# Performance work log

Measured on AMD Instinct MI355X. Metric: run time of the kernel, lower is better.

The kernel has to match this reference:

```python
import jax, jax.numpy as jnp
import numpy as np

G = 2            # num_codevector_groups
C = 320          # num_codevectors_per_group
VQ_DIM = 256     # codevector_dim
HID = 512        # conv_dimensions[-1]
TAU = 2.0


def setup_inputs() -> dict:
    key = jax.random.key(0)
    k1, k2, k3, k4 = jax.random.split(key, 4)
    B, S = 16, 2048
    x = jax.random.normal(k1, (B, S, HID), dtype=jnp.float32)
    # iid Gumbel(0,1) noise, same shape as flattened logits [B*S*G, C]
    u = jax.random.uniform(k2, (B * S * G, C), dtype=jnp.float32, minval=1e-6, maxval=1.0 - 1e-6)
    gumbel = -jnp.log(-jnp.log(u))
    Wq = jax.random.normal(k3, (G * C, HID), dtype=jnp.float32) * (1.0 / np.sqrt(HID))
    bq = jnp.zeros((G * C,), dtype=jnp.float32)
    codevectors = jax.random.uniform(k4, (1, G * C, VQ_DIM // G), dtype=jnp.float32)
    return {"x": x, "gumbel": gumbel, "Wq": Wq, "bq": bq, "codevectors": codevectors}


def reference(x, gumbel, Wq, bq, codevectors):
    B, S, H = x.shape
    N = B * S
    logits = jnp.einsum('bsh,gh->bsg', x, Wq) + bq          # [B, S, G*C]
    logits = logits.reshape(N * G, C)

    # hard gumbel-softmax (training path) with straight-through estimator
    y_soft = jax.nn.softmax((logits + gumbel) / TAU, axis=-1)
    idx = jnp.argmax(y_soft, axis=-1)
    y_hard = jax.nn.one_hot(idx, C, dtype=y_soft.dtype)
    probs = y_hard + y_soft - jax.lax.stop_gradient(y_soft)  # [N*G, C]

    # perplexity from plain softmax of logits (no gumbel noise), masked_token_idx=None
    soft_probs = jax.nn.softmax(logits.reshape(N, G, C), axis=-1)
    mean_p = soft_probs.mean(axis=0)                          # [G, C]
    perplexity = jnp.exp(-jnp.sum(mean_p * jnp.log(mean_p + 1e-7), axis=-1)).sum()

    # weighted sum over codes per group == einsum (same math as broadcast*sum in torch)
    cv = codevectors.reshape(G, C, VQ_DIM // G)               # [G, C, d]
    sel = jnp.einsum('ngc,gcd->ngd', probs.reshape(N, G, C), cv)
    selected_codes = sel.reshape(B, S, VQ_DIM)
    return selected_codes, perplexity
```

## Files before the change

kernel.cpp:

```cpp
#include <hip/hip_runtime.h>
#include <hip/hip_fp16.h>

#define HID 512
#define GC  640
#define CC  320
#define GG  2
#define DHALF 128
#define MARGIN 0.004f
#define FB 4
#define REPLD 324

typedef __attribute__((ext_vector_type(8))) _Float16 half8;
typedef __attribute__((ext_vector_type(4))) float float4v;

__device__ __forceinline__ void gload16(const void* g, void* l) {
    __builtin_amdgcn_global_load_lds(
        (const __attribute__((address_space(1))) void*)(unsigned long long)g,
        (__attribute__((address_space(3))) void*)(unsigned)(unsigned long long)l,
        16, 0, 0);
}

__global__ __launch_bounds__(256) void zero_misc(float* meanAcc, int* cnt) {
    for (int i = threadIdx.x; i < GC; i += 256) meanAcc[i] = 0.f;
    if (threadIdx.x < 2) cnt[threadIdx.x] = 0;
}

__global__ __launch_bounds__(256) void convert_f16(
    const float* __restrict__ in, unsigned short* __restrict__ out, int n8)
{
    int i = blockIdx.x * 256 + threadIdx.x;
    if (i >= n8) return;
    const float4* p = (const float4*)in + (size_t)i * 2;
    float4 v0 = p[0], v1 = p[1];
    float f[8] = {v0.x, v0.y, v0.z, v0.w, v1.x, v1.y, v1.z, v1.w};
    unsigned r[4];
#pragma unroll
    for (int j = 0; j < 4; ++j) {
        __half2 hh = __float22half2_rn(make_float2(f[2*j], f[2*j+1]));
        r[j] = __builtin_bit_cast(unsigned, hh);
    }
    uint4 o = {r[0], r[1], r[2], r[3]};
    *(uint4*)(out + (size_t)i * 8) = o;
}

__global__ __launch_bounds__(512, 4) void fused(
    const float* __restrict__ X, const unsigned short* __restrict__ Wh,
    const float* __restrict__ bq, const float* __restrict__ gum,
    const float* __restrict__ cv, float* __restrict__ out,
    float* __restrict__ meanAcc, int* __restrict__ cnt,
    int* __restrict__ flags0, int* __restrict__ flags1)
{
    __shared__ __align__(16) char lds[49152];
    unsigned short* As0 = (unsigned short*)lds;
    unsigned short* Bs0 = (unsigned short*)(lds + 8192);
    float* rep = (float*)lds;
    __shared__ float bqs[CC];
    __shared__ float smean[CC];

    const int tid  = threadIdx.x;
    const int lane = tid & 63;
    const int wid  = tid >> 6;
    const int wr   = wid >> 1;
    const int wc   = wid & 1;
    const int lq   = lane & 15;
    const int q    = lane >> 4;

    int bid = blockIdx.x, nwg = gridDim.x;
    int swz = ((nwg & 7) == 0) ? (bid & 7) * (nwg >> 3) + (bid >> 3) : bid;
    const int g    = swz & 1;
    const int tok0 = (swz >> 1) * 64;
    int* flagsg = g ? flags1 : flags0;

    for (int i = tid; i < CC; i += 512) { bqs[i] = bq[g * CC + i]; smean[i] = 0.f; }

    const int iss0 = wid, iss1 = wid + 8, iss2 = wid + 16;
    const int c0i = (iss0 * 64 + lane) ^ (((iss0 * 64 + lane) >> 3) & 7);
    const int c1i = (iss1 * 64 + lane) ^ (((iss1 * 64 + lane) >> 3) & 7);
    const int c2i = (iss2 * 64 + lane) ^ (((iss2 * 64 + lane) >> 3) & 7);
    const unsigned short* srcB0 = Wh + ((size_t)(g * CC + (c0i >> 2))) * HID + (c0i & 3) * 8;
    const unsigned short* srcB1 = Wh + ((size_t)(g * CC + (c1i >> 2))) * HID + (c1i & 3) * 8;
    const unsigned short* srcB2 = Wh + ((size_t)(g * CC + (c2i >> 2))) * HID + (c2i & 3) * 8;

    const int ca = tid ^ ((tid >> 3) & 7);
    const float* xsrc = X + (size_t)(tok0 + (ca >> 2)) * HID + (ca & 3) * 8;

    int aoff = ((wr * 16 + lq) << 6) + (q << 4);
    aoff ^= ((aoff >> 7) & 7) << 4;
    int boff = (lq << 6) + (q << 4);
    boff ^= ((lq >> 1) & 7) << 4;
    boff += wc * 10240;

    float4v acc[10];
#pragma unroll
    for (int j = 0; j < 10; ++j) acc[j] = (float4v){0.f, 0.f, 0.f, 0.f};

    if (tid < 256) {
        float4 xa = *(const float4*)xsrc;
        float4 xb = *(const float4*)(xsrc + 4);
        half8 h;
        h[0] = (_Float16)xa.x; h[1] = (_Float16)xa.y;
        h[2] = (_Float16)xa.z; h[3] = (_Float16)xa.w;
        h[4] = (_Float16)xb.x; h[5] = (_Float16)xb.y;
        h[6] = (_Float16)xb.z; h[7] = (_Float16)xb.w;
        *(half8*)&As0[tid * 8] = h;
    }
    gload16(srcB0, Bs0 + iss0 * 512);
    gload16(srcB1, Bs0 + iss1 * 512);
    if (wid < 4) gload16(srcB2, Bs0 + iss2 * 512);
    __syncthreads();

    int cur = 0;
    for (int kk = 0; kk < 16; ++kk) {
        const int k0n = ((kk + 1) & 15) * 32;
        float4 nxa = {}, nxb = {};
        if (tid < 256) {
            nxa = *(const float4*)(xsrc + k0n);
            nxb = *(const float4*)(xsrc + k0n + 4);
        }
        unsigned short* Bnext = Bs0 + (cur ^ 1) * 10240;
        gload16(srcB0 + k0n, Bnext + iss0 * 512);
        gload16(srcB1 + k0n, Bnext + iss1 * 512);
        if (wid < 4) gload16(srcB2 + k0n, Bnext + iss2 * 512);

        half8 a = *(const half8*)((const char*)(As0 + cur * 2048) + aoff);
        const char* bbase = (const char*)(Bs0 + cur * 10240) + boff;
#pragma unroll
        for (int j = 0; j < 10; ++j) {
            half8 b = *(const half8*)(bbase + j * 1024);
            acc[j] = __builtin_amdgcn_mfma_f32_16x16x32_f16(a, b, acc[j], 0, 0, 0);
        }

        if (tid < 256) {
            half8 h;
            h[0] = (_Float16)nxa.x; h[1] = (_Float16)nxa.y;
            h[2] = (_Float16)nxa.z; h[3] = (_Float16)nxa.w;
            h[4] = (_Float16)nxb.x; h[5] = (_Float16)nxb.y;
            h[6] = (_Float16)nxb.z; h[7] = (_Float16)nxb.w;
            *(half8*)&As0[(cur ^ 1) * 2048 + tid * 8] = h;
        }
        __syncthreads();
        cur ^= 1;
    }

    float macc[20];
#pragma unroll
    for (int j = 0; j < 20; ++j) macc[j] = 0.f;
    const int gg  = tid >> 4;
    const int lql = tid & 15;
    const int cb  = lql * 20;

    for (int r = 0; r < 4; ++r) {
        const int slot = wr * 4 + q;
#pragma unroll
        for (int j = 0; j < 10; ++j) {
            const int c = wc * 160 + j * 16 + lq;
            rep[slot * REPLD + c] = acc[j][r] + bqs[c];
        }
        __syncthreads();

        if (gg < 16) {
            const int rowL  = (gg >> 2) * 16 + (gg & 3) * 4 + r;
            const int tglob = tok0 + rowL;
            const float* grow = gum + ((size_t)tglob * GG + g) * CC + cb;
            const float* rrow = rep + gg * REPLD + cb;

            float s = 0.f;
            float b = -3.0e38f; int bi = 0; float s2 = -3.0e38f;
#pragma unroll
            for (int jj = 0; jj < 5; ++jj) {
                float4 lv = *(const float4*)(rrow + jj * 4);
                float4 gv = *(const float4*)(grow + jj * 4);
                float lf[4] = {lv.x, lv.y, lv.z, lv.w};
                float gf[4] = {gv.x, gv.y, gv.z, gv.w};
#pragma unroll
                for (int t = 0; t < 4; ++t) {
                    float v = lf[t] + gf[t];
                    if (v > b)       { s2 = b; b = v; bi = cb + jj * 4 + t; }
                    else if (v > s2) { s2 = v; }
                    s += __expf(lf[t]);
                }
            }
#pragma unroll
            for (int m = 1; m < 16; m <<= 1) {
                float os  = __shfl_xor(s,  m, 64);
                float ob  = __shfl_xor(b,  m, 64);
                int   obi = __shfl_xor(bi, m, 64);
                float os2 = __shfl_xor(s2, m, 64);
                s += os;
                if (ob > b || (ob == b && obi < bi)) { s2 = fmaxf(os2, b); b = ob; bi = obi; }
                else                                 { s2 = fmaxf(s2, ob); }
            }
            float inv = 1.f / s;
#pragma unroll
            for (int jj = 0; jj < 5; ++jj) {
                float4 lv = *(const float4*)(rrow + jj * 4);
                macc[jj*4+0] += __expf(lv.x) * inv;
                macc[jj*4+1] += __expf(lv.y) * inv;
                macc[jj*4+2] += __expf(lv.z) * inv;
                macc[jj*4+3] += __expf(lv.w) * inv;
            }

            if (lql == 0 && (b - s2) < MARGIN) {
                int p = atomicAdd(&cnt[g], 1);
                flagsg[p] = tglob;
            }
            const float* cvp = cv + ((size_t)(g * CC + bi)) * DHALF + lql * 8;
            float4 c0v = *(const float4*)cvp;
            float4 c1v = *(const float4*)(cvp + 4);
            float* op = out + (size_t)tglob * 256 + g * DHALF + lql * 8;
            *(float4*)op       = c0v;
            *(float4*)(op + 4) = c1v;
        }
        __syncthreads();
    }

    if (tid < 256) {
#pragma unroll
        for (int j = 0; j < 20; ++j)
            atomicAdd(&smean[cb + j], macc[j]);
    }
    __syncthreads();
    for (int i = tid; i < CC; i += 512)
        atomicAdd(&meanAcc[g * CC + i], smean[i]);
}

__global__ __launch_bounds__(320) void fixup(
    const float* __restrict__ X, const float* __restrict__ W,
    const float* __restrict__ bq, const float* __restrict__ gum,
    const float* __restrict__ cv, float* __restrict__ out,
    const int* __restrict__ flags0, const int* __restrict__ flags1,
    const int* __restrict__ cnt)
{
    __shared__ float xs[FB][HID];
    __shared__ float vals[FB][CC];
    __shared__ int stok[FB];
    const int tid = threadIdx.x;
    const int n0 = cnt[0], n1 = cnt[1];
    const int nb0 = (n0 + FB - 1) / FB;
    const int nb1 = (n1 + FB - 1) / FB;

    for (int bb = blockIdx.x; bb < nb0 + nb1; bb += gridDim.x) {
        const int g    = (bb < nb0) ? 0 : 1;
        const int lb   = (bb < nb0) ? bb : bb - nb0;
        const int n    = g ? n1 : n0;
        const int* fl  = g ? flags1 : flags0;
        const int r0   = lb * FB;
        const int nr   = (n - r0 < FB) ? (n - r0) : FB;

        if (tid < FB) {
            int idx = r0 + tid;
            if (idx >= n) idx = n - 1;
            stok[tid] = fl[idx];
        }
        __syncthreads();
        for (int i = tid; i < FB * (HID / 4); i += 320) {
            int r = i >> 7, k4 = i & 127;
            *(float4*)&xs[r][k4 * 4] = *(const float4*)(X + (size_t)stok[r] * HID + k4 * 4);
        }
        __syncthreads();

        {
            const int c = tid;
            if (c < CC) {
                const float* wr = W + (size_t)(g * CC + c) * HID;
                float acc[FB];
#pragma unroll
                for (int r = 0; r < FB; ++r) acc[r] = 0.f;
                for (int k4 = 0; k4 < HID / 4; ++k4) {
                    float4 w4 = *(const float4*)(wr + k4 * 4);
#pragma unroll
                    for (int r = 0; r < FB; ++r) {
                        float4 xv = *(const float4*)&xs[r][k4 * 4];
                        acc[r] = fmaf(xv.x, w4.x, acc[r]);
                        acc[r] = fmaf(xv.y, w4.y, acc[r]);
                        acc[r] = fmaf(xv.z, w4.z, acc[r]);
                        acc[r] = fmaf(xv.w, w4.w, acc[r]);
                    }
                }
                float bias = bq[g * CC + c];
#pragma unroll
                for (int r = 0; r < FB; ++r)
                    vals[r][c] = acc[r] + bias + gum[((size_t)stok[r] * GG + g) * CC + c];
            }
        }
        __syncthreads();

        const int lane = tid & 63;
        const int wv   = tid >> 6;
        if (wv < FB) {
            const int r = wv;
            if (r < nr) {
                float b = -3.0e38f; int bi = 0;
#pragma unroll
                for (int j = 0; j < 5; ++j) {
                    int c = lane + j * 64;
                    float v = vals[r][c];
                    if (v > b || (v == b && c < bi)) { b = v; bi = c; }
                }
#pragma unroll
                for (int m = 32; m; m >>= 1) {
                    float ob = __shfl_xor(b, m, 64);
                    int  obi = __shfl_xor(bi, m, 64);
                    if (ob > b || (ob == b && obi < bi)) { b = ob; bi = obi; }
                }
                int tok = stok[r];
                float2 cvv = *(const float2*)(cv + ((size_t)(g * CC + bi)) * DHALF + lane * 2);
                *(float2*)(out + (size_t)tok * 256 + g * DHALF + lane * 2) = cvv;
            }
        }
        __syncthreads();
    }
}

__global__ __launch_bounds__(256) void perpk(
    const float* __restrict__ meanAcc, float* __restrict__ outp, int ntot)
{
    __shared__ float red0[256];
    __shared__ float red1[256];
    const float invn = 1.f / (float)ntot;
    float h0 = 0.f, h1 = 0.f;
    for (int c = threadIdx.x; c < CC; c += 256) {
        float p0 = meanAcc[c]      * invn;
        float p1 = meanAcc[CC + c] * invn;
        h0 -= p0 * logf(p0 + 1e-7f);
        h1 -= p1 * logf(p1 + 1e-7f);
    }
    red0[threadIdx.x] = h0; red1[threadIdx.x] = h1;
    __syncthreads();
    for (int s = 128; s; s >>= 1) {
        if (threadIdx.x < (unsigned)s) {
            red0[threadIdx.x] += red0[threadIdx.x + s];
            red1[threadIdx.x] += red1[threadIdx.x + s];
        }
        __syncthreads();
    }
    if (threadIdx.x == 0) outp[0] = expf(red0[0]) + expf(red1[0]);
}

extern "C" void kernel_launch(void* const* d_in, const int* in_sizes, int n_in,
                              void* d_out, int out_size, void* d_ws, size_t ws_size,
                              hipStream_t stream) {
    const float* x      = (const float*)d_in[0];
    const float* gumbel = (const float*)d_in[1];
    const float* Wq     = (const float*)d_in[2];
    const float* bq     = (const float*)d_in[3];
    const float* cv     = (const float*)d_in[4];
    float* out = (float*)d_out;

    const int NT = in_sizes[0] / HID;

    char* wsc = (char*)d_ws;
    float* meanAcc = (float*)wsc;
    int*   cnt     = (int*)(wsc + 2560);
    int*   flags0  = (int*)(wsc + 4096);
    int*   flags1  = (int*)(wsc + 135168);
    unsigned short* Wh = (unsigned short*)(wsc + 266240);

    zero_misc<<<1, 256, 0, stream>>>(meanAcc, cnt);
    convert_f16<<<(GC * HID / 8 + 255) / 256, 256, 0, stream>>>(Wq, Wh, GC * HID / 8);

    const int nwg = (NT / 64) * 2;
    fused<<<nwg, 512, 0, stream>>>(x, Wh, bq, gumbel, cv, out,
                                   meanAcc, cnt, flags0, flags1);

    fixup<<<256, 320, 0, stream>>>(x, Wq, bq, gumbel, cv, out, flags0, flags1, cnt);
    perpk<<<1, 256, 0, stream>>>(meanAcc, out + (size_t)out_size - 1, NT);
}
```

Baseline: 125.6 us.

## Triple-buffer weight tiles and load X straight into registers in fused GEMM

```diff
diff --git a/kernel.cpp b/kernel.cpp
--- a/kernel.cpp
+++ b/kernel.cpp
@@ -8,7 +8,6 @@
 #define DHALF 128
 #define MARGIN 0.004f
 #define FB 4
-#define REPLD 324
 
 typedef __attribute__((ext_vector_type(8))) _Float16 half8;
 typedef __attribute__((ext_vector_type(4))) float float4v;
@@ -18,6 +17,15 @@
         (const __attribute__((address_space(1))) void*)(unsigned long long)g,
         (__attribute__((address_space(3))) void*)(unsigned)(unsigned long long)l,
         16, 0, 0);
+}
+
+__device__ __forceinline__ half8 cvt8(float4 a, float4 b) {
+    half8 h;
+    h[0] = (_Float16)a.x; h[1] = (_Float16)a.y;
+    h[2] = (_Float16)a.z; h[3] = (_Float16)a.w;
+    h[4] = (_Float16)b.x; h[5] = (_Float16)b.y;
+    h[6] = (_Float16)b.z; h[7] = (_Float16)b.w;
+    return h;
 }
 
 __global__ __launch_bounds__(256) void zero_misc(float* meanAcc, int* cnt) {
@@ -43,27 +51,23 @@
     *(uint4*)(out + (size_t)i * 8) = o;
 }
 
-__global__ __launch_bounds__(512, 4) void fused(
+__global__ __launch_bounds__(512, 2) void fused(
     const float* __restrict__ X, const unsigned short* __restrict__ Wh,
     const float* __restrict__ bq, const float* __restrict__ gum,
     const float* __restrict__ cv, float* __restrict__ out,
     float* __restrict__ meanAcc, int* __restrict__ cnt,
     int* __restrict__ flags0, int* __restrict__ flags1)
 {
-    __shared__ __align__(16) char lds[49152];
-    unsigned short* As0 = (unsigned short*)lds;
-    unsigned short* Bs0 = (unsigned short*)(lds + 8192);
-    float* rep = (float*)lds;
+    __shared__ __align__(16) char smemc[61440];
     __shared__ float bqs[CC];
-    __shared__ float smean[CC];
+    float* rep   = (float*)smemc;
+    float* smean = (float*)(smemc + 40960);
 
     const int tid  = threadIdx.x;
     const int lane = tid & 63;
     const int wid  = tid >> 6;
-    const int wr   = wid >> 1;
-    const int wc   = wid & 1;
-    const int lq   = lane & 15;
-    const int q    = lane >> 4;
+    const int wr   = wid >> 1, wc = wid & 1;
+    const int lq   = lane & 15, q = lane >> 4;
 
     int bid = blockIdx.x, nwg = gridDim.x;
     int swz = ((nwg & 7) == 0) ? (bid & 7) * (nwg >> 3) + (bid >> 3) : bid;
@@ -71,90 +75,102 @@
     const int tok0 = (swz >> 1) * 64;
     int* flagsg = g ? flags1 : flags0;
 
-    for (int i = tid; i < CC; i += 512) { bqs[i] = bq[g * CC + i]; smean[i] = 0.f; }
-
-    const int iss0 = wid, iss1 = wid + 8, iss2 = wid + 16;
-    const int c0i = (iss0 * 64 + lane) ^ (((iss0 * 64 + lane) >> 3) & 7);
-    const int c1i = (iss1 * 64 + lane) ^ (((iss1 * 64 + lane) >> 3) & 7);
-    const int c2i = (iss2 * 64 + lane) ^ (((iss2 * 64 + lane) >> 3) & 7);
-    const unsigned short* srcB0 = Wh + ((size_t)(g * CC + (c0i >> 2))) * HID + (c0i & 3) * 8;
-    const unsigned short* srcB1 = Wh + ((size_t)(g * CC + (c1i >> 2))) * HID + (c1i & 3) * 8;
-    const unsigned short* srcB2 = Wh + ((size_t)(g * CC + (c2i >> 2))) * HID + (c2i & 3) * 8;
-
-    const int ca = tid ^ ((tid >> 3) & 7);
-    const float* xsrc = X + (size_t)(tok0 + (ca >> 2)) * HID + (ca & 3) * 8;
-
-    int aoff = ((wr * 16 + lq) << 6) + (q << 4);
-    aoff ^= ((aoff >> 7) & 7) << 4;
-    int boff = (lq << 6) + (q << 4);
-    boff ^= ((lq >> 1) & 7) << 4;
-    boff += wc * 10240;
+    for (int i = tid; i < CC; i += 512) bqs[i] = bq[g * CC + i];
+
+    const int nb = (wid < 4) ? 3 : 2;
+    int sl[3];
+    if (wid < 4) { sl[0] = wid * 3; sl[1] = sl[0] + 1; sl[2] = sl[0] + 2; }
+    else         { sl[0] = 12 + (wid - 4) * 2; sl[1] = sl[0] + 1; sl[2] = sl[0]; }
+    const unsigned short* bsrcp[3];
+#pragma unroll
+    for (int u = 0; u < 3; ++u) {
+        int c = sl[u] * 64 + lane;
+        int kc = c / 320, row = c - kc * 320;
+        bsrcp[u] = Wh + ((size_t)(g * CC + row)) * HID + kc * 8;
+    }
+    const float* xsrc = X + (size_t)(tok0 + wr * 16 + lq) * HID + q * 8;
 
     float4v acc[10];
 #pragma unroll
     for (int j = 0; j < 10; ++j) acc[j] = (float4v){0.f, 0.f, 0.f, 0.f};
 
-    if (tid < 256) {
-        float4 xa = *(const float4*)xsrc;
-        float4 xb = *(const float4*)(xsrc + 4);
-        half8 h;
-        h[0] = (_Float16)xa.x; h[1] = (_Float16)xa.y;
-        h[2] = (_Float16)xa.z; h[3] = (_Float16)xa.w;
-        h[4] = (_Float16)xb.x; h[5] = (_Float16)xb.y;
-        h[6] = (_Float16)xb.z; h[7] = (_Float16)xb.w;
-        *(half8*)&As0[tid * 8] = h;
-    }
-    gload16(srcB0, Bs0 + iss0 * 512);
-    gload16(srcB1, Bs0 + iss1 * 512);
-    if (wid < 4) gload16(srcB2, Bs0 + iss2 * 512);
+    auto issueB = [&](int kstep) {
+        unsigned short* dbase = (unsigned short*)(smemc + (kstep % 3) * 20480);
+#pragma unroll
+        for (int u = 0; u < 3; ++u)
+            if (u < nb) gload16(bsrcp[u] + kstep * 32, dbase + sl[u] * 512);
+    };
+    auto compute10 = [&](int buf, half8 a) {
+        const char* bb = smemc + buf * 20480 + q * 5120 + wc * 2560 + lq * 16;
+#pragma unroll
+        for (int j = 0; j < 10; ++j) {
+            half8 b = *(const half8*)(bb + j * 256);
+            acc[j] = __builtin_amdgcn_mfma_f32_16x16x32_f16(a, b, acc[j], 0, 0, 0);
+        }
+    };
+
+    float4 nxa = *(const float4*)xsrc;
+    float4 nxb = *(const float4*)(xsrc + 4);
+    issueB(0);
+    __builtin_amdgcn_sched_barrier(0);
+    issueB(1);
+
+    if (wid < 4) asm volatile("s_waitcnt vmcnt(3)" ::: "memory");
+    else         asm volatile("s_waitcnt vmcnt(2)" ::: "memory");
+    __builtin_amdgcn_s_barrier();
+    __builtin_amdgcn_sched_barrier(0);
+    {
+        half8 a = cvt8(nxa, nxb);
+        nxa = *(const float4*)(xsrc + 32);
+        nxb = *(const float4*)(xsrc + 36);
+        issueB(2);
+        compute10(0, a);
+    }
+
+    for (int kk = 1; kk <= 13; ++kk) {
+        if (wid < 4) asm volatile("s_waitcnt vmcnt(5)" ::: "memory");
+        else         asm volatile("s_waitcnt vmcnt(4)" ::: "memory");
+        __builtin_amdgcn_s_barrier();
+        __builtin_amdgcn_sched_barrier(0);
+        half8 a = cvt8(nxa, nxb);
+        nxa = *(const float4*)(xsrc + (kk + 1) * 32);
+        nxb = *(const float4*)(xsrc + (kk + 1) * 32 + 4);
+        issueB(kk + 2);
+        compute10(kk % 3, a);
+    }
+
+    if (wid < 4) asm volatile("s_waitcnt vmcnt(5)" ::: "memory");
+    else         asm volatile("s_waitcnt vmcnt(4)" ::: "memory");
+    __builtin_amdgcn_s_barrier();
+    __builtin_amdgcn_sched_barrier(0);
+    {
+        half8 a = cvt8(nxa, nxb);
+        nxa = *(const float4*)(xsrc + 15 * 32);
+        nxb = *(const float4*)(xsrc + 15 * 32 + 4);
+        compute10(2, a);
+    }
+
+    asm volatile("s_waitcnt vmcnt(2)" ::: "memory");
+    __builtin_amdgcn_s_barrier();
+    __builtin_amdgcn_sched_barrier(0);
+    {
+        half8 a = cvt8(nxa, nxb);
+        compute10(0, a);
+    }
     __syncthreads();
 
-    int cur = 0;
-    for (int kk = 0; kk < 16; ++kk) {
-        const int k0n = ((kk + 1) & 15) * 32;
-        float4 nxa = {}, nxb = {};
-        if (tid < 256) {
-            nxa = *(const float4*)(xsrc + k0n);
-            nxb = *(const float4*)(xsrc + k0n + 4);
-        }
-        unsigned short* Bnext = Bs0 + (cur ^ 1) * 10240;
-        gload16(srcB0 + k0n, Bnext + iss0 * 512);
-        gload16(srcB1 + k0n, Bnext + iss1 * 512);
-        if (wid < 4) gload16(srcB2 + k0n, Bnext + iss2 * 512);
-
-        half8 a = *(const half8*)((const char*)(As0 + cur * 2048) + aoff);
-        const char* bbase = (const char*)(Bs0 + cur * 10240) + boff;
-#pragma unroll
-        for (int j = 0; j < 10; ++j) {
-            half8 b = *(const half8*)(bbase + j * 1024);
-            acc[j] = __builtin_amdgcn_mfma_f32_16x16x32_f16(a, b, acc[j], 0, 0, 0);
-        }
-
-        if (tid < 256) {
-            half8 h;
-            h[0] = (_Float16)nxa.x; h[1] = (_Float16)nxa.y;
-            h[2] = (_Float16)nxa.z; h[3] = (_Float16)nxa.w;
-            h[4] = (_Float16)nxb.x; h[5] = (_Float16)nxb.y;
-            h[6] = (_Float16)nxb.z; h[7] = (_Float16)nxb.w;
-            *(half8*)&As0[(cur ^ 1) * 2048 + tid * 8] = h;
-        }
-        __syncthreads();
-        cur ^= 1;
-    }
-
     float macc[20];
 #pragma unroll
     for (int j = 0; j < 20; ++j) macc[j] = 0.f;
-    const int gg  = tid >> 4;
-    const int lql = tid & 15;
-    const int cb  = lql * 20;
-
+    const int gg = tid >> 4, lql = tid & 15, cb = lql * 20;
+
+#pragma unroll
     for (int r = 0; r < 4; ++r) {
         const int slot = wr * 4 + q;
 #pragma unroll
         for (int j = 0; j < 10; ++j) {
             const int c = wc * 160 + j * 16 + lq;
-            rep[slot * REPLD + c] = acc[j][r] + bqs[c];
+            rep[slot * 324 + c] = acc[j][r] + bqs[c];
         }
         __syncthreads();
 
@@ -162,7 +178,7 @@
             const int rowL  = (gg >> 2) * 16 + (gg & 3) * 4 + r;
             const int tglob = tok0 + rowL;
             const float* grow = gum + ((size_t)tglob * GG + g) * CC + cb;
-            const float* rrow = rep + gg * REPLD + cb;
+            const float* rrow = rep + gg * 324 + cb;
 
             float s = 0.f;
             float b = -3.0e38f; int bi = 0; float s2 = -3.0e38f;
@@ -214,6 +230,8 @@
         __syncthreads();
     }
 
+    for (int i = tid; i < CC; i += 512) smean[i] = 0.f;
+    __syncthreads();
     if (tid < 256) {
 #pragma unroll
         for (int j = 0; j < 20; ++j)
@@ -286,9 +304,9 @@
         __syncthreads();
 
         const int lane = tid & 63;
-        const int wv   = tid >> 6;
-        if (wv < FB) {
-            const int r = wv;
+        const int wvv  = tid >> 6;
+        if (wvv < FB) {
+            const int r = wvv;
             if (r < nr) {
                 float b = -3.0e38f; int bi = 0;
 #pragma unroll
```

Result: slower. 171.8 us (+36.8%).
